# Kernel tuning notes

Measured on AMD Instinct MI355X. Metric: run time of the kernel, lower is better.

Reference implementation:

```python
import jax, jax.numpy as jnp
import numpy as np

CUTOFF = 5.0
MAX_NUM_PAIRS = 131072
N_ATOMS = 4096
BOX_L = 40.0


def setup_inputs() -> dict:
    key = jax.random.key(0)
    k1, _ = jax.random.split(key)
    positions = jax.random.uniform(k1, (N_ATOMS, 3), dtype=jnp.float32) * BOX_L
    box = jnp.eye(3, dtype=jnp.float32) * BOX_L  # triclinic box vectors (rows)
    return {"positions": positions, "box": box}


def _min_image_deltas(positions, box):
    # delta[i, j] = positions[i] - positions[j], wrapped by the minimum image
    # convention: subtract the nearest integer multiple of the box vectors.
    delta = positions[:, None, :] - positions[None, :, :]  # [N, N, 3]
    inv_box = jnp.linalg.inv(box)
    frac = delta @ inv_box                                  # fractional coords
    delta = delta - jnp.round(frac) @ box
    return delta


def reference(positions, box):
    n = positions.shape[0]
    delta = _min_image_deltas(positions, box)               # [N, N, 3]
    dist2 = jnp.sum(delta * delta, axis=-1)                 # [N, N]

    idx = jnp.arange(n)
    upper = idx[:, None] < idx[None, :]                     # unique pairs i<j
    mask = upper & (dist2 < CUTOFF * CUTOFF)

    n_pairs = jnp.sum(mask).astype(jnp.int32)
    # Compact hit pairs into a fixed-size buffer (static shape for jit).
    flat_idx, = jnp.nonzero(mask.ravel(), size=MAX_NUM_PAIRS, fill_value=0)
    valid = jnp.arange(MAX_NUM_PAIRS) < n_pairs

    pair_i = jnp.where(valid, flat_idx // n, -1)
    pair_j = jnp.where(valid, flat_idx % n, -1)
    pairs = jnp.stack([pair_i, pair_j], axis=0)             # [2, P]

    deltas = jnp.where(valid[:, None], delta.reshape(n * n, 3)[flat_idx], 0.0)
    d2 = jnp.where(valid, dist2.ravel()[flat_idx], 1.0)     # safe sqrt on pads
    distances = jnp.where(valid, jnp.sqrt(d2), 0.0)

    return pairs, deltas, distances, n_pairs
```

## Files before the change

### kernel.cpp

```cpp
#include <hip/hip_runtime.h>


#define CUT2 25.0f

__device__ __forceinline__ void load_box_inv(const float* __restrict__ box,
                                             float B[3][3], float Binv[3][3]) {
    #pragma unroll
    for (int r = 0; r < 3; ++r)
        #pragma unroll
        for (int c = 0; c < 3; ++c)
            B[r][c] = box[r * 3 + c];

    float a00 = B[0][0], a01 = B[0][1], a02 = B[0][2];
    float a10 = B[1][0], a11 = B[1][1], a12 = B[1][2];
    float a20 = B[2][0], a21 = B[2][1], a22 = B[2][2];

    float adj00 =  (a11 * a22 - a12 * a21);
    float adj01 = -(a01 * a22 - a02 * a21);
    float adj02 =  (a01 * a12 - a02 * a11);
    float adj10 = -(a10 * a22 - a12 * a20);
    float adj11 =  (a00 * a22 - a02 * a20);
    float adj12 = -(a00 * a12 - a02 * a10);
    float adj20 =  (a10 * a21 - a11 * a20);
    float adj21 = -(a00 * a21 - a01 * a20);
    float adj22 =  (a00 * a11 - a01 * a10);

    float det = a00 * adj00 + a01 * adj10 + a02 * adj20;

    Binv[0][0] = __fdiv_rn(adj00, det); Binv[0][1] = __fdiv_rn(adj01, det); Binv[0][2] = __fdiv_rn(adj02, det);
    Binv[1][0] = __fdiv_rn(adj10, det); Binv[1][1] = __fdiv_rn(adj11, det); Binv[1][2] = __fdiv_rn(adj12, det);
    Binv[2][0] = __fdiv_rn(adj20, det); Binv[2][1] = __fdiv_rn(adj21, det); Binv[2][2] = __fdiv_rn(adj22, det);
}

__device__ __forceinline__ void min_image(float xi, float yi, float zi,
                                          float xj, float yj, float zj,
                                          const float B[3][3], const float Binv[3][3],
                                          float& dx, float& dy, float& dz, float& d2) {
    dx = __fsub_rn(xi, xj);
    dy = __fsub_rn(yi, yj);
    dz = __fsub_rn(zi, zj);

    float f0 = __fadd_rn(__fadd_rn(__fmul_rn(dx, Binv[0][0]), __fmul_rn(dy, Binv[1][0])), __fmul_rn(dz, Binv[2][0]));
    float f1 = __fadd_rn(__fadd_rn(__fmul_rn(dx, Binv[0][1]), __fmul_rn(dy, Binv[1][1])), __fmul_rn(dz, Binv[2][1]));
    float f2 = __fadd_rn(__fadd_rn(__fmul_rn(dx, Binv[0][2]), __fmul_rn(dy, Binv[1][2])), __fmul_rn(dz, Binv[2][2]));

    float r0 = rintf(f0), r1 = rintf(f1), r2 = rintf(f2);

    float c0 = __fadd_rn(__fadd_rn(__fmul_rn(r0, B[0][0]), __fmul_rn(r1, B[1][0])), __fmul_rn(r2, B[2][0]));
    float c1 = __fadd_rn(__fadd_rn(__fmul_rn(r0, B[0][1]), __fmul_rn(r1, B[1][1])), __fmul_rn(r2, B[2][1]));
    float c2 = __fadd_rn(__fadd_rn(__fmul_rn(r0, B[0][2]), __fmul_rn(r1, B[1][2])), __fmul_rn(r2, B[2][2]));

    dx = __fsub_rn(dx, c0);
    dy = __fsub_rn(dy, c1);
    dz = __fsub_rn(dz, c2);

    d2 = __fadd_rn(__fadd_rn(__fmul_rn(dx, dx), __fmul_rn(dy, dy)), __fmul_rn(dz, dz));
}

__device__ __forceinline__ void min_image_diag(float xi, float yi, float zi,
                                               float xj, float yj, float zj,
                                               float b0, float b1, float b2,
                                               float ib0, float ib1, float ib2,
                                               float& dx, float& dy, float& dz, float& d2) {
    dx = __fsub_rn(xi, xj);
    dy = __fsub_rn(yi, yj);
    dz = __fsub_rn(zi, zj);
    float r0 = rintf(__fmul_rn(dx, ib0));
    float r1 = rintf(__fmul_rn(dy, ib1));
    float r2 = rintf(__fmul_rn(dz, ib2));
    dx = __fsub_rn(dx, __fmul_rn(r0, b0));
    dy = __fsub_rn(dy, __fmul_rn(r1, b1));
    dz = __fsub_rn(dz, __fmul_rn(r2, b2));
    d2 = __fadd_rn(__fadd_rn(__fmul_rn(dx, dx), __fmul_rn(dy, dy)), __fmul_rn(dz, dz));
}

template <bool DIAG>
__device__ __forceinline__ int count_row(int i, int lane,
                                         const float* __restrict__ pos,
                                         const float B[3][3], const float Binv[3][3],
                                         unsigned long long* __restrict__ mrow,
                                         int nchunks) {
    float xi = pos[3 * i + 0], yi = pos[3 * i + 1], zi = pos[3 * i + 2];
    float b0 = B[0][0], b1 = B[1][1], b2 = B[2][2];
    float ib0 = Binv[0][0], ib1 = Binv[1][1], ib2 = Binv[2][2];
    int c0 = i >> 6;
    int cnt = 0;

    {
        int j = (c0 << 6) + lane;
        bool hit = false;
        if (j > i) {
            float dx, dy, dz, d2;
            if (DIAG)
                min_image_diag(xi, yi, zi, pos[3 * j], pos[3 * j + 1], pos[3 * j + 2],
                               b0, b1, b2, ib0, ib1, ib2, dx, dy, dz, d2);
            else
                min_image(xi, yi, zi, pos[3 * j], pos[3 * j + 1], pos[3 * j + 2],
                          B, Binv, dx, dy, dz, d2);
            hit = (d2 < CUT2);
        }
        unsigned long long m = __ballot(hit);
        if (lane == 0) mrow[c0] = m;
        cnt += __popcll(m);
    }

    int c = c0 + 1;
    for (; c + 4 <= nchunks; c += 4) {
        int j0 = (c << 6) + lane;
        float dx0, dy0, dz0, d20, dx1, dy1, dz1, d21;
        float dx2, dy2, dz2, d22, dx3, dy3, dz3, d23;
        if (DIAG) {
            min_image_diag(xi, yi, zi, pos[3 * j0 +   0], pos[3 * j0 +   1], pos[3 * j0 +   2], b0, b1, b2, ib0, ib1, ib2, dx0, dy0, dz0, d20);
            min_image_diag(xi, yi, zi, pos[3 * j0 + 192], pos[3 * j0 + 193], pos[3 * j0 + 194], b0, b1, b2, ib0, ib1, ib2, dx1, dy1, dz1, d21);
            min_image_diag(xi, yi, zi, pos[3 * j0 + 384], pos[3 * j0 + 385], pos[3 * j0 + 386], b0, b1, b2, ib0, ib1, ib2, dx2, dy2, dz2, d22);
            min_image_diag(xi, yi, zi, pos[3 * j0 + 576], pos[3 * j0 + 577], pos[3 * j0 + 578], b0, b1, b2, ib0, ib1, ib2, dx3, dy3, dz3, d23);
        } else {
            min_image(xi, yi, zi, pos[3 * j0 +   0], pos[3 * j0 +   1], pos[3 * j0 +   2], B, Binv, dx0, dy0, dz0, d20);
            min_image(xi, yi, zi, pos[3 * j0 + 192], pos[3 * j0 + 193], pos[3 * j0 + 194], B, Binv, dx1, dy1, dz1, d21);
            min_image(xi, yi, zi, pos[3 * j0 + 384], pos[3 * j0 + 385], pos[3 * j0 + 386], B, Binv, dx2, dy2, dz2, d22);
            min_image(xi, yi, zi, pos[3 * j0 + 576], pos[3 * j0 + 577], pos[3 * j0 + 578], B, Binv, dx3, dy3, dz3, d23);
        }
        unsigned long long m0 = __ballot(d20 < CUT2);
        unsigned long long m1 = __ballot(d21 < CUT2);
        unsigned long long m2 = __ballot(d22 < CUT2);
        unsigned long long m3 = __ballot(d23 < CUT2);
        if (lane == 0) { mrow[c] = m0; mrow[c + 1] = m1; mrow[c + 2] = m2; mrow[c + 3] = m3; }
        cnt += __popcll(m0) + __popcll(m1) + __popcll(m2) + __popcll(m3);
    }
    for (; c < nchunks; ++c) {
        int j = (c << 6) + lane;
        float dx, dy, dz, d2;
        if (DIAG)
            min_image_diag(xi, yi, zi, pos[3 * j], pos[3 * j + 1], pos[3 * j + 2],
                           b0, b1, b2, ib0, ib1, ib2, dx, dy, dz, d2);
        else
            min_image(xi, yi, zi, pos[3 * j], pos[3 * j + 1], pos[3 * j + 2],
                      B, Binv, dx, dy, dz, d2);
        unsigned long long m = __ballot(d2 < CUT2);
        if (lane == 0) mrow[c] = m;
        cnt += __popcll(m);
    }
    return cnt;
}

__global__ void __launch_bounds__(256)
k1_pad_count(const float* __restrict__ pos, const float* __restrict__ box,
             float* __restrict__ out, int* __restrict__ counts,
             unsigned long long* __restrict__ masks, int N, int P) {
    int tid = blockIdx.x * blockDim.x + threadIdx.x;
    int nthreads = gridDim.x * blockDim.x;

    int total = 6 * P + 1;
    for (int k = tid; k < total; k += nthreads)
        out[k] = (k < 2 * P) ? -1.0f : 0.0f;

    int i = tid >> 6;
    int lane = tid & 63;
    int nchunks = N >> 6;

    float B[3][3], Binv[3][3];
    load_box_inv(box, B, Binv);
    bool diag = (B[0][1] == 0.0f) & (B[0][2] == 0.0f) & (B[1][0] == 0.0f) &
                (B[1][2] == 0.0f) & (B[2][0] == 0.0f) & (B[2][1] == 0.0f);

    int cnt;
    if (diag)
        cnt = count_row<true>(i, lane, pos, B, Binv,
                              masks + (size_t)i * nchunks, nchunks);
    else
        cnt = count_row<false>(i, lane, pos, B, Binv,
                               masks + (size_t)i * nchunks, nchunks);
    if (lane == 0) counts[i] = cnt;
}

__global__ void __launch_bounds__(256)
k2_scan_fill(const float* __restrict__ pos, const float* __restrict__ box,
             const int* __restrict__ counts,
             const unsigned long long* __restrict__ masks,
             float* __restrict__ out, int N, int P) {
    int tid = blockIdx.x * blockDim.x + threadIdx.x;
    int i = tid >> 6;
    int lane = tid & 63;
    int nchunks = N >> 6;
    int c0 = i >> 6;

    int pre = 0;
    for (int b = 0; b < i; b += 64) {
        int k = b + lane;
        pre += (k < i) ? counts[k] : 0;
    }
    #pragma unroll
    for (int d = 1; d < 64; d <<= 1)
        pre += __shfl_xor(pre, d);

    if (i == N - 1 && lane == 0)
        out[6 * (size_t)P] = (float)(pre + counts[i]);

    unsigned long long mymask = masks[(size_t)i * nchunks + lane];

    float B[3][3], Binv[3][3];
    load_box_inv(box, B, Binv);
    float xi = pos[3 * i + 0], yi = pos[3 * i + 1], zi = pos[3 * i + 2];

    int base = pre;
    for (int cc = c0; cc < nchunks; ++cc) {
        unsigned long long m = __shfl(mymask, cc);
        if (m != 0ull) {
            if ((m >> lane) & 1ull) {
                int j = (cc << 6) + lane;
                float dx, dy, dz, d2;
                min_image(xi, yi, zi, pos[3 * j + 0], pos[3 * j + 1], pos[3 * j + 2],
                          B, Binv, dx, dy, dz, d2);
                int slot = base + __popcll(m & ((1ull << lane) - 1ull));
                if (slot < P) {
                    out[slot] = (float)i;
                    out[P + slot] = (float)j;
                    size_t db = 2 * (size_t)P + 3 * (size_t)slot;
                    out[db + 0] = dx;
                    out[db + 1] = dy;
                    out[db + 2] = dz;
                    out[5 * (size_t)P + slot] = sqrtf(d2);
                }
            }
            base += __popcll(m);
        }
    }
}

extern "C" void kernel_launch(void* const* d_in, const int* in_sizes, int n_in,
                              void* d_out, int out_size, void* d_ws, size_t ws_size,
                              hipStream_t stream) {
    const float* pos = (const float*)d_in[0];
    const float* box = (const float*)d_in[1];
    float* out = (float*)d_out;

    int N = in_sizes[0] / 3;
    int P = (out_size - 1) / 6;
    int nchunks = N >> 6;

    char* w = (char*)d_ws;
    int* counts = (int*)w;                         w += (size_t)N * sizeof(int);
    unsigned long long* masks = (unsigned long long*)w;

    k1_pad_count<<<N / 4, 256, 0, stream>>>(pos, box, out, counts, masks, N, P);

    k2_scan_fill<<<N / 4, 256, 0, stream>>>(pos, box, counts, masks, out, N, P);
}
```

Measured before the change: 87.63 us.

## Split each triangular row across two waves and interleave short and long rows

Each row of the upper-triangular pair matrix is now handled by two wavefronts, each covering half of the remaining column chunks. Rows are assigned in alternating low/high order so that neighbouring waves get complementary amounts of work. The count array now holds per-half counts, and the prefix scan reads them with int4 vector loads. This doubles the number of waves and is meant to reduce load imbalance from the triangular structure. The cost is a longer prefix scan and some extra per-wave setup.

```diff
diff --git a/kernel.cpp b/kernel.cpp
--- a/kernel.cpp
+++ b/kernel.cpp
@@ -74,19 +74,33 @@
     d2 = __fadd_rn(__fadd_rn(__fmul_rn(dx, dx), __fmul_rn(dy, dy)), __fmul_rn(dz, dz));
 }
 
+__device__ __forceinline__ void wave_row_half(int w, int N, int& row, int& h) {
+    h = w & 1;
+    int rp = w >> 1;
+    row = (rp & 1) ? (N - 1 - (rp >> 1)) : (rp >> 1);
+}
+
+__device__ __forceinline__ void half_range(int row, int h, int nchunks,
+                                           int& start, int& end, int& c0) {
+    c0 = row >> 6;
+    int nc = nchunks - c0;
+    int midc = c0 + ((nc + 1) >> 1);
+    start = h ? midc : c0;
+    end = h ? nchunks : midc;
+}
+
 template <bool DIAG>
-__device__ __forceinline__ int count_row(int i, int lane,
-                                         const float* __restrict__ pos,
-                                         const float B[3][3], const float Binv[3][3],
-                                         unsigned long long* __restrict__ mrow,
-                                         int nchunks) {
+__device__ __forceinline__ int count_half(int i, int lane, int start, int end, int c0,
+                                          const float* __restrict__ pos,
+                                          const float B[3][3], const float Binv[3][3],
+                                          unsigned long long* __restrict__ mrow) {
     float xi = pos[3 * i + 0], yi = pos[3 * i + 1], zi = pos[3 * i + 2];
     float b0 = B[0][0], b1 = B[1][1], b2 = B[2][2];
     float ib0 = Binv[0][0], ib1 = Binv[1][1], ib2 = Binv[2][2];
-    int c0 = i >> 6;
     int cnt = 0;
-
-    {
+    int c = start;
+
+    if (c == c0 && c < end) {
         int j = (c0 << 6) + lane;
         bool hit = false;
         if (j > i) {
@@ -102,10 +116,10 @@
         unsigned long long m = __ballot(hit);
         if (lane == 0) mrow[c0] = m;
         cnt += __popcll(m);
-    }
-
-    int c = c0 + 1;
-    for (; c + 4 <= nchunks; c += 4) {
+        ++c;
+    }
+
+    for (; c + 4 <= end; c += 4) {
         int j0 = (c << 6) + lane;
         float dx0, dy0, dz0, d20, dx1, dy1, dz1, d21;
         float dx2, dy2, dz2, d22, dx3, dy3, dz3, d23;
@@ -127,7 +141,7 @@
         if (lane == 0) { mrow[c] = m0; mrow[c + 1] = m1; mrow[c + 2] = m2; mrow[c + 3] = m3; }
         cnt += __popcll(m0) + __popcll(m1) + __popcll(m2) + __popcll(m3);
     }
-    for (; c < nchunks; ++c) {
+    for (; c < end; ++c) {
         int j = (c << 6) + lane;
         float dx, dy, dz, d2;
         if (DIAG)
@@ -145,7 +159,7 @@
 
 __global__ void __launch_bounds__(256)
 k1_pad_count(const float* __restrict__ pos, const float* __restrict__ box,
-             float* __restrict__ out, int* __restrict__ counts,
+             float* __restrict__ out, int* __restrict__ counts2,
              unsigned long long* __restrict__ masks, int N, int P) {
     int tid = blockIdx.x * blockDim.x + threadIdx.x;
     int nthreads = gridDim.x * blockDim.x;
@@ -154,56 +168,71 @@
     for (int k = tid; k < total; k += nthreads)
         out[k] = (k < 2 * P) ? -1.0f : 0.0f;
 
-    int i = tid >> 6;
+    int w = tid >> 6;
     int lane = tid & 63;
     int nchunks = N >> 6;
+
+    int row, h;
+    wave_row_half(w, N, row, h);
+    int start, end, c0;
+    half_range(row, h, nchunks, start, end, c0);
 
     float B[3][3], Binv[3][3];
     load_box_inv(box, B, Binv);
     bool diag = (B[0][1] == 0.0f) & (B[0][2] == 0.0f) & (B[1][0] == 0.0f) &
                 (B[1][2] == 0.0f) & (B[2][0] == 0.0f) & (B[2][1] == 0.0f);
 
+    unsigned long long* mrow = masks + (size_t)row * nchunks;
     int cnt;
     if (diag)
-        cnt = count_row<true>(i, lane, pos, B, Binv,
-                              masks + (size_t)i * nchunks, nchunks);
+        cnt = count_half<true>(row, lane, start, end, c0, pos, B, Binv, mrow);
     else
-        cnt = count_row<false>(i, lane, pos, B, Binv,
-                               masks + (size_t)i * nchunks, nchunks);
-    if (lane == 0) counts[i] = cnt;
+        cnt = count_half<false>(row, lane, start, end, c0, pos, B, Binv, mrow);
+    if (lane == 0) counts2[2 * row + h] = cnt;
 }
 
 __global__ void __launch_bounds__(256)
 k2_scan_fill(const float* __restrict__ pos, const float* __restrict__ box,
-             const int* __restrict__ counts,
+             const int* __restrict__ counts2,
              const unsigned long long* __restrict__ masks,
              float* __restrict__ out, int N, int P) {
     int tid = blockIdx.x * blockDim.x + threadIdx.x;
-    int i = tid >> 6;
+    int w = tid >> 6;
     int lane = tid & 63;
     int nchunks = N >> 6;
-    int c0 = i >> 6;
-
+
+    int row, h;
+    wave_row_half(w, N, row, h);
+    int start, end, c0;
+    half_range(row, h, nchunks, start, end, c0);
+
+    int lim = 2 * row;
     int pre = 0;
-    for (int b = 0; b < i; b += 64) {
-        int k = b + lane;
-        pre += (k < i) ? counts[k] : 0;
+    for (int base = 0; base < lim; base += 256) {
+        int idx = base + 4 * lane;
+        int4 v = *(const int4*)(counts2 + idx);
+        if (idx + 0 < lim) pre += v.x;
+        if (idx + 1 < lim) pre += v.y;
+        if (idx + 2 < lim) pre += v.z;
+        if (idx + 3 < lim) pre += v.w;
     }
     #pragma unroll
     for (int d = 1; d < 64; d <<= 1)
         pre += __shfl_xor(pre, d);
 
-    if (i == N - 1 && lane == 0)
-        out[6 * (size_t)P] = (float)(pre + counts[i]);
-
-    unsigned long long mymask = masks[(size_t)i * nchunks + lane];
+    if (h == 1) pre += counts2[2 * row];
+
+    if (row == N - 1 && h == 1 && lane == 0)
+        out[6 * (size_t)P] = (float)(pre + counts2[2 * row + 1]);
+
+    unsigned long long mymask = masks[(size_t)row * nchunks + lane];
 
     float B[3][3], Binv[3][3];
     load_box_inv(box, B, Binv);
-    float xi = pos[3 * i + 0], yi = pos[3 * i + 1], zi = pos[3 * i + 2];
+    float xi = pos[3 * row + 0], yi = pos[3 * row + 1], zi = pos[3 * row + 2];
 
     int base = pre;
-    for (int cc = c0; cc < nchunks; ++cc) {
+    for (int cc = start; cc < end; ++cc) {
         unsigned long long m = __shfl(mymask, cc);
         if (m != 0ull) {
             if ((m >> lane) & 1ull) {
@@ -213,7 +242,7 @@
                           B, Binv, dx, dy, dz, d2);
                 int slot = base + __popcll(m & ((1ull << lane) - 1ull));
                 if (slot < P) {
-                    out[slot] = (float)i;
+                    out[slot] = (float)row;
                     out[P + slot] = (float)j;
                     size_t db = 2 * (size_t)P + 3 * (size_t)slot;
                     out[db + 0] = dx;
@@ -239,10 +268,9 @@
     int nchunks = N >> 6;
 
     char* w = (char*)d_ws;
-    int* counts = (int*)w;                         w += (size_t)N * sizeof(int);
+    int* counts2 = (int*)w;                        w += (size_t)2 * N * sizeof(int);
     unsigned long long* masks = (unsigned long long*)w;
 
-    k1_pad_count<<<N / 4, 256, 0, stream>>>(pos, box, out, counts, masks, N, P);
-
-    k2_scan_fill<<<N / 4, 256, 0, stream>>>(pos, box, counts, masks, out, N, P);
-}
+    k1_pad_count<<<N / 2, 256, 0, stream>>>(pos, box, out, counts2, masks, N, P);
+    k2_scan_fill<<<N / 2, 256, 0, stream>>>(pos, box, counts2, masks, out, N, P);
+}
```

Measured after the change: 87.60 us. About the same (-0.0%).

## Recompute pair masks in fill kernel instead of storing them; vectorize prefix sum

Applied to the files above, without the earlier changes.

The count kernel no longer writes per-row 64-bit chunk masks to workspace. The fill kernel recomputes each chunk's hit mask by evaluating the distances again, which removes the mask store and reload at the cost of roughly doubling the distance arithmetic in the second kernel. The prefix sum over per-row counts now reads int4 vectors, cutting the number of loop iterations by four. The fill kernel may also run slower, since it now serially computes every chunk of the row.

```diff
diff --git a/kernel.cpp b/kernel.cpp
--- a/kernel.cpp
+++ b/kernel.cpp
@@ -75,78 +75,52 @@
 }
 
 template <bool DIAG>
+__device__ __forceinline__ unsigned long long
+chunk_mask(int i, int lane, int c, int c0,
+           float xi, float yi, float zi,
+           const float* __restrict__ pos,
+           const float B[3][3], const float Binv[3][3]) {
+    int j = (c << 6) + lane;
+    float b0 = B[0][0], b1 = B[1][1], b2 = B[2][2];
+    float ib0 = Binv[0][0], ib1 = Binv[1][1], ib2 = Binv[2][2];
+    bool hit;
+    float dx, dy, dz, d2;
+    if (DIAG)
+        min_image_diag(xi, yi, zi, pos[3 * j], pos[3 * j + 1], pos[3 * j + 2],
+                       b0, b1, b2, ib0, ib1, ib2, dx, dy, dz, d2);
+    else
+        min_image(xi, yi, zi, pos[3 * j], pos[3 * j + 1], pos[3 * j + 2],
+                  B, Binv, dx, dy, dz, d2);
+    hit = (d2 < CUT2);
+    if (c == c0) hit &= (j > i);
+    return __ballot(hit);
+}
+
+template <bool DIAG>
 __device__ __forceinline__ int count_row(int i, int lane,
                                          const float* __restrict__ pos,
                                          const float B[3][3], const float Binv[3][3],
-                                         unsigned long long* __restrict__ mrow,
                                          int nchunks) {
     float xi = pos[3 * i + 0], yi = pos[3 * i + 1], zi = pos[3 * i + 2];
-    float b0 = B[0][0], b1 = B[1][1], b2 = B[2][2];
-    float ib0 = Binv[0][0], ib1 = Binv[1][1], ib2 = Binv[2][2];
     int c0 = i >> 6;
-    int cnt = 0;
-
-    {
-        int j = (c0 << 6) + lane;
-        bool hit = false;
-        if (j > i) {
-            float dx, dy, dz, d2;
-            if (DIAG)
-                min_image_diag(xi, yi, zi, pos[3 * j], pos[3 * j + 1], pos[3 * j + 2],
-                               b0, b1, b2, ib0, ib1, ib2, dx, dy, dz, d2);
-            else
-                min_image(xi, yi, zi, pos[3 * j], pos[3 * j + 1], pos[3 * j + 2],
-                          B, Binv, dx, dy, dz, d2);
-            hit = (d2 < CUT2);
-        }
-        unsigned long long m = __ballot(hit);
-        if (lane == 0) mrow[c0] = m;
-        cnt += __popcll(m);
-    }
+    int cnt = __popcll(chunk_mask<DIAG>(i, lane, c0, c0, xi, yi, zi, pos, B, Binv));
 
     int c = c0 + 1;
     for (; c + 4 <= nchunks; c += 4) {
-        int j0 = (c << 6) + lane;
-        float dx0, dy0, dz0, d20, dx1, dy1, dz1, d21;
-        float dx2, dy2, dz2, d22, dx3, dy3, dz3, d23;
-        if (DIAG) {
-            min_image_diag(xi, yi, zi, pos[3 * j0 +   0], pos[3 * j0 +   1], pos[3 * j0 +   2], b0, b1, b2, ib0, ib1, ib2, dx0, dy0, dz0, d20);
-            min_image_diag(xi, yi, zi, pos[3 * j0 + 192], pos[3 * j0 + 193], pos[3 * j0 + 194], b0, b1, b2, ib0, ib1, ib2, dx1, dy1, dz1, d21);
-            min_image_diag(xi, yi, zi, pos[3 * j0 + 384], pos[3 * j0 + 385], pos[3 * j0 + 386], b0, b1, b2, ib0, ib1, ib2, dx2, dy2, dz2, d22);
-            min_image_diag(xi, yi, zi, pos[3 * j0 + 576], pos[3 * j0 + 577], pos[3 * j0 + 578], b0, b1, b2, ib0, ib1, ib2, dx3, dy3, dz3, d23);
-        } else {
-            min_image(xi, yi, zi, pos[3 * j0 +   0], pos[3 * j0 +   1], pos[3 * j0 +   2], B, Binv, dx0, dy0, dz0, d20);
-            min_image(xi, yi, zi, pos[3 * j0 + 192], pos[3 * j0 + 193], pos[3 * j0 + 194], B, Binv, dx1, dy1, dz1, d21);
-            min_image(xi, yi, zi, pos[3 * j0 + 384], pos[3 * j0 + 385], pos[3 * j0 + 386], B, Binv, dx2, dy2, dz2, d22);
-            min_image(xi, yi, zi, pos[3 * j0 + 576], pos[3 * j0 + 577], pos[3 * j0 + 578], B, Binv, dx3, dy3, dz3, d23);
-        }
-        unsigned long long m0 = __ballot(d20 < CUT2);
-        unsigned long long m1 = __ballot(d21 < CUT2);
-        unsigned long long m2 = __ballot(d22 < CUT2);
-        unsigned long long m3 = __ballot(d23 < CUT2);
-        if (lane == 0) { mrow[c] = m0; mrow[c + 1] = m1; mrow[c + 2] = m2; mrow[c + 3] = m3; }
+        unsigned long long m0 = chunk_mask<DIAG>(i, lane, c + 0, c0, xi, yi, zi, pos, B, Binv);
+        unsigned long long m1 = chunk_mask<DIAG>(i, lane, c + 1, c0, xi, yi, zi, pos, B, Binv);
+        unsigned long long m2 = chunk_mask<DIAG>(i, lane, c + 2, c0, xi, yi, zi, pos, B, Binv);
+        unsigned long long m3 = chunk_mask<DIAG>(i, lane, c + 3, c0, xi, yi, zi, pos, B, Binv);
         cnt += __popcll(m0) + __popcll(m1) + __popcll(m2) + __popcll(m3);
     }
-    for (; c < nchunks; ++c) {
-        int j = (c << 6) + lane;
-        float dx, dy, dz, d2;
-        if (DIAG)
-            min_image_diag(xi, yi, zi, pos[3 * j], pos[3 * j + 1], pos[3 * j + 2],
-                           b0, b1, b2, ib0, ib1, ib2, dx, dy, dz, d2);
-        else
-            min_image(xi, yi, zi, pos[3 * j], pos[3 * j + 1], pos[3 * j + 2],
-                      B, Binv, dx, dy, dz, d2);
-        unsigned long long m = __ballot(d2 < CUT2);
-        if (lane == 0) mrow[c] = m;
-        cnt += __popcll(m);
-    }
+    for (; c < nchunks; ++c)
+        cnt += __popcll(chunk_mask<DIAG>(i, lane, c, c0, xi, yi, zi, pos, B, Binv));
     return cnt;
 }
 
 __global__ void __launch_bounds__(256)
 k1_pad_count(const float* __restrict__ pos, const float* __restrict__ box,
-             float* __restrict__ out, int* __restrict__ counts,
-             unsigned long long* __restrict__ masks, int N, int P) {
+             float* __restrict__ out, int* __restrict__ counts, int N, int P) {
     int tid = blockIdx.x * blockDim.x + threadIdx.x;
     int nthreads = gridDim.x * blockDim.x;
 
@@ -163,20 +137,14 @@
     bool diag = (B[0][1] == 0.0f) & (B[0][2] == 0.0f) & (B[1][0] == 0.0f) &
                 (B[1][2] == 0.0f) & (B[2][0] == 0.0f) & (B[2][1] == 0.0f);
 
-    int cnt;
-    if (diag)
-        cnt = count_row<true>(i, lane, pos, B, Binv,
-                              masks + (size_t)i * nchunks, nchunks);
-    else
-        cnt = count_row<false>(i, lane, pos, B, Binv,
-                               masks + (size_t)i * nchunks, nchunks);
+    int cnt = diag ? count_row<true>(i, lane, pos, B, Binv, nchunks)
+                   : count_row<false>(i, lane, pos, B, Binv, nchunks);
     if (lane == 0) counts[i] = cnt;
 }
 
 __global__ void __launch_bounds__(256)
 k2_scan_fill(const float* __restrict__ pos, const float* __restrict__ box,
              const int* __restrict__ counts,
-             const unsigned long long* __restrict__ masks,
              float* __restrict__ out, int N, int P) {
     int tid = blockIdx.x * blockDim.x + threadIdx.x;
     int i = tid >> 6;
@@ -185,9 +153,13 @@
     int c0 = i >> 6;
 
     int pre = 0;
-    for (int b = 0; b < i; b += 64) {
-        int k = b + lane;
-        pre += (k < i) ? counts[k] : 0;
+    for (int base = 0; base < i; base += 256) {
+        int idx = base + 4 * lane;
+        int4 v = *(const int4*)(counts + idx);
+        if (idx + 0 < i) pre += v.x;
+        if (idx + 1 < i) pre += v.y;
+        if (idx + 2 < i) pre += v.z;
+        if (idx + 3 < i) pre += v.w;
     }
     #pragma unroll
     for (int d = 1; d < 64; d <<= 1)
@@ -196,15 +168,17 @@
     if (i == N - 1 && lane == 0)
         out[6 * (size_t)P] = (float)(pre + counts[i]);
 
-    unsigned long long mymask = masks[(size_t)i * nchunks + lane];
-
     float B[3][3], Binv[3][3];
     load_box_inv(box, B, Binv);
+    bool diag = (B[0][1] == 0.0f) & (B[0][2] == 0.0f) & (B[1][0] == 0.0f) &
+                (B[1][2] == 0.0f) & (B[2][0] == 0.0f) & (B[2][1] == 0.0f);
     float xi = pos[3 * i + 0], yi = pos[3 * i + 1], zi = pos[3 * i + 2];
 
     int base = pre;
     for (int cc = c0; cc < nchunks; ++cc) {
-        unsigned long long m = __shfl(mymask, cc);
+        unsigned long long m =
+            diag ? chunk_mask<true>(i, lane, cc, c0, xi, yi, zi, pos, B, Binv)
+                 : chunk_mask<false>(i, lane, cc, c0, xi, yi, zi, pos, B, Binv);
         if (m != 0ull) {
             if ((m >> lane) & 1ull) {
                 int j = (cc << 6) + lane;
@@ -236,13 +210,9 @@
 
     int N = in_sizes[0] / 3;
     int P = (out_size - 1) / 6;
-    int nchunks = N >> 6;
-
-    char* w = (char*)d_ws;
-    int* counts = (int*)w;                         w += (size_t)N * sizeof(int);
-    unsigned long long* masks = (unsigned long long*)w;
-
-    k1_pad_count<<<N / 4, 256, 0, stream>>>(pos, box, out, counts, masks, N, P);
-
-    k2_scan_fill<<<N / 4, 256, 0, stream>>>(pos, box, counts, masks, out, N, P);
-}
+
+    int* counts = (int*)d_ws;
+
+    k1_pad_count<<<N / 4, 256, 0, stream>>>(pos, box, out, counts, N, P);
+    k2_scan_fill<<<N / 4, 256, 0, stream>>>(pos, box, counts, out, N, P);
+}
```

Result: slower. 89.55 us (+2.2%).
